# Kernel optimization log

Hardware: AMD Instinct MI355X
Metric: run time of the kernel (lower is better)

## Reference

```python
import jax, jax.numpy as jnp
import numpy as np

S, B, H = 2048, 32, 1024


def setup_inputs() -> dict:
    key = jax.random.key(0)
    k1, k2, k3, k4, k5 = jax.random.split(key, 5)
    scale_w = 1.0 / np.sqrt(2 * H)
    return {
        "hidden": jax.random.normal(k1, (1, B, H), dtype=jnp.float32),
        "encoder_outputs": jax.random.normal(k2, (S, B, H), dtype=jnp.float32),
        "W_attn": jax.random.normal(k3, (H, 2 * H), dtype=jnp.float32) * scale_w,
        "b_attn": jax.random.normal(k4, (H,), dtype=jnp.float32) * scale_w,
        "v": jax.random.normal(k5, (H,), dtype=jnp.float32) * (1.0 / np.sqrt(H)),
    }


def reference(hidden, encoder_outputs, W_attn, b_attn, v):
    # hidden: [1, B, H], encoder_outputs: [S, B, H]
    h = jnp.broadcast_to(hidden, encoder_outputs.shape)          # [S, B, H]
    cat = jnp.concatenate([h, encoder_outputs], axis=2)          # [S, B, 2H]
    alphas = jnp.tanh(jnp.einsum('sbk,hk->sbh', cat, W_attn) + b_attn)  # [S, B, H]
    scores = jnp.einsum('sbh,h->sb', alphas, v)                  # [S, B]
    # softmax over source positions S per batch row, output [B, 1, S]
    return jax.nn.softmax(scores.T, axis=1)[:, None, :]
```

## Files before the change

### kernel.cpp

```cpp
#include <hip/hip_runtime.h>
#include <hip/hip_bf16.h>

typedef unsigned short u16;
typedef unsigned long long u64;
typedef __bf16 bf16x8 __attribute__((ext_vector_type(8)));
typedef float f32x4 __attribute__((ext_vector_type(4)));

#define S_DIM 2048
#define B_DIM 32
#define H_DIM 1024
#define M_DIM (S_DIM * B_DIM)
#define BM 64
#define BKS 32
#define NKS (H_DIM / BKS)

__device__ __forceinline__ float fast_tanh(float x) {
  float e = __expf(2.0f * x);
  return 1.0f - 2.0f * __builtin_amdgcn_rcpf(e + 1.0f);
}

__device__ __forceinline__ void gload_lds16(const void* g, void* l) {
  __builtin_amdgcn_global_load_lds(
      (const __attribute__((address_space(1))) unsigned int*)g,
      (__attribute__((address_space(3))) unsigned int*)l,
      16, 0, 0);
}

__global__ void wconv_kernel(const float* __restrict__ W, u16* __restrict__ W2) {
  const int h = blockIdx.x;
  const int t = threadIdx.x;
  float4 w4 = *(const float4*)(W + (size_t)h * (2 * H_DIM) + H_DIM + t * 4);
  union { u16 s[4]; uint2 v; } pk;
  pk.s[0] = __builtin_bit_cast(u16, (__bf16)w4.x);
  pk.s[1] = __builtin_bit_cast(u16, (__bf16)w4.y);
  pk.s[2] = __builtin_bit_cast(u16, (__bf16)w4.z);
  pk.s[3] = __builtin_bit_cast(u16, (__bf16)w4.w);
  *(uint2*)(W2 + (size_t)h * H_DIM + t * 4) = pk.v;
}

__global__ void uprep_kernel(const float* __restrict__ hidden, const float* __restrict__ W,
                             const float* __restrict__ bias, float* __restrict__ u) {
  int t = blockIdx.x * 256 + threadIdx.x;
  int h = t >> 7;
  int b = (t >> 2) & 31;
  int kq = t & 3;
  const float4* hv = (const float4*)(hidden + (size_t)b * H_DIM) + kq * 64;
  const float4* wv = (const float4*)(W + (size_t)h * (2 * H_DIM)) + kq * 64;
  float acc = 0.f;
  #pragma unroll 4
  for (int i = 0; i < 64; ++i) {
    float4 a = hv[i], w = wv[i];
    acc += a.x * w.x + a.y * w.y + a.z * w.z + a.w * w.w;
  }
  acc += __shfl_xor(acc, 1);
  acc += __shfl_xor(acc, 2);
  if (kq == 0) u[(size_t)b * H_DIM + h] = acc + bias[h];
}

__launch_bounds__(512, 2)
__global__ void gemm_kernel(const float* __restrict__ enc, const u16* __restrict__ W2,
                            const float* __restrict__ u, const float* __restrict__ v,
                            float* __restrict__ scores) {
  __shared__ u16 A_s[2][BM][40];
  __shared__ u16 B_s[2][H_DIM * BKS];
  __shared__ float red_s[8][BM];

  const int tid  = threadIdx.x;
  const int lane = tid & 63;
  const int wid  = tid >> 6;
  const int q    = lane >> 4;
  const int c16  = lane & 15;
  const int n0   = wid * 128;
  const int m0   = blockIdx.x * BM;

  const int ar  = tid >> 3;
  const int acf = tid & 7;
  const float* aptr = enc + (size_t)(m0 + ar) * H_DIM + acf * 4;

  f32x4 acc[4][8];
  #pragma unroll
  for (int mi = 0; mi < 4; ++mi)
    #pragma unroll
    for (int nf = 0; nf < 8; ++nf) {
      f32x4 z = {0.f, 0.f, 0.f, 0.f};
      acc[mi][nf] = z;
    }

  #define STAGE_B(buf, ks)                                                     \
    {                                                                          \
      _Pragma("unroll")                                                        \
      for (int j = 0; j < 8; ++j) {                                            \
        const int L16 = j * 512 + tid;                                         \
        const int h   = L16 >> 2;                                              \
        const int cp  = L16 & 3;                                               \
        const int c   = cp ^ ((h >> 1) & 3);                                   \
        gload_lds16(W2 + (size_t)h * H_DIM + (ks) * BKS + c * 8,               \
                    &B_s[buf][L16 * 8]);                                       \
      }                                                                        \
    }

  #define WRITE_A(buf, f4)                                                     \
    {                                                                          \
      union { u16 s[4]; u64 v; } pk;                                           \
      pk.s[0] = __builtin_bit_cast(u16, (__bf16)(f4).x);                       \
      pk.s[1] = __builtin_bit_cast(u16, (__bf16)(f4).y);                       \
      pk.s[2] = __builtin_bit_cast(u16, (__bf16)(f4).z);                       \
      pk.s[3] = __builtin_bit_cast(u16, (__bf16)(f4).w);                       \
      *(u64*)&A_s[buf][ar][acf * 4] = pk.v;                                    \
    }

  STAGE_B(0, 0);
  {
    float4 a0 = *(const float4*)(aptr);
    WRITE_A(0, a0);
  }
  __syncthreads();

  #pragma unroll 2
  for (int ks = 0; ks < NKS; ++ks) {
    const int cur = ks & 1;
    const int nxt = cur ^ 1;
    float4 av;
    if (ks + 1 < NKS) {
      STAGE_B(nxt, ks + 1);
      av = *(const float4*)(aptr + (ks + 1) * BKS);
    }
    bf16x8 a[4], b[8];
    #pragma unroll
    for (int mi = 0; mi < 4; ++mi)
      a[mi] = *(const bf16x8*)&A_s[cur][mi * 16 + c16][q * 8];
    #pragma unroll
    for (int nf = 0; nf < 8; ++nf) {
      const int col = n0 + nf * 16 + c16;
      b[nf] = *(const bf16x8*)&B_s[cur][col * BKS + ((q ^ ((col >> 1) & 3)) * 8)];
    }
    #pragma unroll
    for (int nf = 0; nf < 8; ++nf)
      #pragma unroll
      for (int mi = 0; mi < 4; ++mi)
        acc[mi][nf] = __builtin_amdgcn_mfma_f32_16x16x32_bf16(a[mi], b[nf], acc[mi][nf], 0, 0, 0);
    if (ks + 1 < NKS) WRITE_A(nxt, av);
    __syncthreads();
  }

  float rowsum[4][4];
  #pragma unroll
  for (int mi = 0; mi < 4; ++mi)
    #pragma unroll
    for (int r = 0; r < 4; ++r) rowsum[mi][r] = 0.f;

  #pragma unroll
  for (int nf = 0; nf < 8; ++nf) {
    const int h = n0 + nf * 16 + c16;
    const float vh = v[h];
    float uv[2][4];
    #pragma unroll
    for (int p = 0; p < 2; ++p)
      #pragma unroll
      for (int r = 0; r < 4; ++r)
        uv[p][r] = u[(size_t)(p * 16 + q * 4 + r) * H_DIM + h];
    #pragma unroll
    for (int mi = 0; mi < 4; ++mi)
      #pragma unroll
      for (int r = 0; r < 4; ++r) {
        float x = acc[mi][nf][r] + uv[mi & 1][r];
        rowsum[mi][r] += vh * fast_tanh(x);
      }
  }
  #pragma unroll
  for (int mi = 0; mi < 4; ++mi)
    #pragma unroll
    for (int r = 0; r < 4; ++r) {
      float s = rowsum[mi][r];
      s += __shfl_xor(s, 1);
      s += __shfl_xor(s, 2);
      s += __shfl_xor(s, 4);
      s += __shfl_xor(s, 8);
      if (c16 == 0) red_s[wid][mi * 16 + q * 4 + r] = s;
    }
  __syncthreads();
  if (tid < BM) {
    float s = 0.f;
    #pragma unroll
    for (int w = 0; w < 8; ++w) s += red_s[w][tid];
    scores[m0 + tid] = s;
  }
  #undef STAGE_B
  #undef WRITE_A
}

__global__ void softmax_kernel(const float* __restrict__ scores, float* __restrict__ out) {
  const int b = blockIdx.x;
  const int t = threadIdx.x;
  const int lane = t & 63, wid = t >> 6;
  __shared__ float redm[4], reds[4];
  float loc[8];
  float mx = -3.0e38f;
  #pragma unroll
  for (int i = 0; i < 8; ++i) {
    loc[i] = scores[(size_t)(i * 256 + t) * B_DIM + b];
    mx = fmaxf(mx, loc[i]);
  }
  #pragma unroll
  for (int off = 1; off < 64; off <<= 1) mx = fmaxf(mx, __shfl_xor(mx, off));
  if (lane == 0) redm[wid] = mx;
  __syncthreads();
  mx = fmaxf(fmaxf(redm[0], redm[1]), fmaxf(redm[2], redm[3]));
  float sum = 0.f;
  #pragma unroll
  for (int i = 0; i < 8; ++i) { loc[i] = __expf(loc[i] - mx); sum += loc[i]; }
  #pragma unroll
  for (int off = 1; off < 64; off <<= 1) sum += __shfl_xor(sum, off);
  if (lane == 0) reds[wid] = sum;
  __syncthreads();
  sum = reds[0] + reds[1] + reds[2] + reds[3];
  float inv = 1.0f / sum;
  #pragma unroll
  for (int i = 0; i < 8; ++i) out[(size_t)b * S_DIM + i * 256 + t] = loc[i] * inv;
}

extern "C" void kernel_launch(void* const* d_in, const int* in_sizes, int n_in,
                              void* d_out, int out_size, void* d_ws, size_t ws_size,
                              hipStream_t stream) {
  const float* hidden = (const float*)d_in[0];
  const float* enc    = (const float*)d_in[1];
  const float* W      = (const float*)d_in[2];
  const float* bias   = (const float*)d_in[3];
  const float* v      = (const float*)d_in[4];
  float* out = (float*)d_out;

  char* ws = (char*)d_ws;
  u16*   W2     = (u16*)ws;
  float* u      = (float*)(ws + (2u << 20));
  float* scores = (float*)(ws + (2u << 20) + (128u << 10));

  wconv_kernel<<<H_DIM, 256, 0, stream>>>(W, W2);
  uprep_kernel<<<512, 256, 0, stream>>>(hidden, W, bias, u);
  gemm_kernel<<<M_DIM / BM, 512, 0, stream>>>(enc, W2, u, v, scores);
  softmax_kernel<<<B_DIM, 256, 0, stream>>>(scores, out);
}
```

Measured before the change: 279.3 us.

## Load W tiles directly into registers instead of staging through LDS

The B operand (bf16 weights) is no longer staged through a 128KB double-buffered LDS array via global_load_lds. Each wave now loads its own B fragments straight from global memory into registers, double-buffered in two register sets. The loop is manually unrolled by two so the register buffers swap at compile time. This cuts LDS traffic and footprint, which may allow more occupancy, but it adds register pressure and issues non-shared global loads. The W tile is re-read per wave and per block, so it depends on L2/L1 hits.

```diff
diff --git a/kernel.cpp b/kernel.cpp
--- a/kernel.cpp
+++ b/kernel.cpp
@@ -17,13 +17,6 @@
 __device__ __forceinline__ float fast_tanh(float x) {
   float e = __expf(2.0f * x);
   return 1.0f - 2.0f * __builtin_amdgcn_rcpf(e + 1.0f);
-}
-
-__device__ __forceinline__ void gload_lds16(const void* g, void* l) {
-  __builtin_amdgcn_global_load_lds(
-      (const __attribute__((address_space(1))) unsigned int*)g,
-      (__attribute__((address_space(3))) unsigned int*)l,
-      16, 0, 0);
 }
 
 __global__ void wconv_kernel(const float* __restrict__ W, u16* __restrict__ W2) {
@@ -62,7 +55,6 @@
                             const float* __restrict__ u, const float* __restrict__ v,
                             float* __restrict__ scores) {
   __shared__ u16 A_s[2][BM][40];
-  __shared__ u16 B_s[2][H_DIM * BKS];
   __shared__ float red_s[8][BM];
 
   const int tid  = threadIdx.x;
@@ -77,6 +69,8 @@
   const int acf = tid & 7;
   const float* aptr = enc + (size_t)(m0 + ar) * H_DIM + acf * 4;
 
+  const u16* wbase = W2 + (size_t)(n0 + c16) * H_DIM + q * 8;
+
   f32x4 acc[4][8];
   #pragma unroll
   for (int mi = 0; mi < 4; ++mi)
@@ -86,17 +80,11 @@
       acc[mi][nf] = z;
     }
 
-  #define STAGE_B(buf, ks)                                                     \
+  #define LOADB(dst, ks)                                                       \
     {                                                                          \
       _Pragma("unroll")                                                        \
-      for (int j = 0; j < 8; ++j) {                                            \
-        const int L16 = j * 512 + tid;                                         \
-        const int h   = L16 >> 2;                                              \
-        const int cp  = L16 & 3;                                               \
-        const int c   = cp ^ ((h >> 1) & 3);                                   \
-        gload_lds16(W2 + (size_t)h * H_DIM + (ks) * BKS + c * 8,               \
-                    &B_s[buf][L16 * 8]);                                       \
-      }                                                                        \
+      for (int nf = 0; nf < 8; ++nf)                                           \
+        dst[nf] = *(const bf16x8*)(wbase + (size_t)nf * 16 * H_DIM + (ks) * BKS); \
     }
 
   #define WRITE_A(buf, f4)                                                     \
@@ -109,38 +97,40 @@
       *(u64*)&A_s[buf][ar][acf * 4] = pk.v;                                    \
     }
 
-  STAGE_B(0, 0);
+  #define KSTEP(ks, BUFC, BCUR, BNXT)                                          \
+    {                                                                          \
+      float4 av;                                                               \
+      const bool pf = (ks) + 1 < NKS;                                          \
+      if (pf) {                                                                \
+        LOADB(BNXT, (ks) + 1);                                                 \
+        av = *(const float4*)(aptr + ((ks) + 1) * BKS);                        \
+      }                                                                        \
+      bf16x8 a[4];                                                             \
+      _Pragma("unroll")                                                        \
+      for (int mi = 0; mi < 4; ++mi)                                           \
+        a[mi] = *(const bf16x8*)&A_s[BUFC][mi * 16 + c16][q * 8];              \
+      _Pragma("unroll")                                                        \
+      for (int nf = 0; nf < 8; ++nf)                                           \
+        _Pragma("unroll")                                                      \
+        for (int mi = 0; mi < 4; ++mi)                                         \
+          acc[mi][nf] = __builtin_amdgcn_mfma_f32_16x16x32_bf16(               \
+              a[mi], BCUR[nf], acc[mi][nf], 0, 0, 0);                          \
+      if (pf) WRITE_A((BUFC) ^ 1, av);                                         \
+      __syncthreads();                                                         \
+    }
+
+  bf16x8 breg0[8], breg1[8];
+  LOADB(breg0, 0);
   {
     float4 a0 = *(const float4*)(aptr);
     WRITE_A(0, a0);
   }
   __syncthreads();
 
-  #pragma unroll 2
-  for (int ks = 0; ks < NKS; ++ks) {
-    const int cur = ks & 1;
-    const int nxt = cur ^ 1;
-    float4 av;
-    if (ks + 1 < NKS) {
-      STAGE_B(nxt, ks + 1);
-      av = *(const float4*)(aptr + (ks + 1) * BKS);
-    }
-    bf16x8 a[4], b[8];
-    #pragma unroll
-    for (int mi = 0; mi < 4; ++mi)
-      a[mi] = *(const bf16x8*)&A_s[cur][mi * 16 + c16][q * 8];
-    #pragma unroll
-    for (int nf = 0; nf < 8; ++nf) {
-      const int col = n0 + nf * 16 + c16;
-      b[nf] = *(const bf16x8*)&B_s[cur][col * BKS + ((q ^ ((col >> 1) & 3)) * 8)];
-    }
-    #pragma unroll
-    for (int nf = 0; nf < 8; ++nf)
-      #pragma unroll
-      for (int mi = 0; mi < 4; ++mi)
-        acc[mi][nf] = __builtin_amdgcn_mfma_f32_16x16x32_bf16(a[mi], b[nf], acc[mi][nf], 0, 0, 0);
-    if (ks + 1 < NKS) WRITE_A(nxt, av);
-    __syncthreads();
+  for (int ks2 = 0; ks2 < NKS / 2; ++ks2) {
+    const int ks = ks2 * 2;
+    KSTEP(ks, 0, breg0, breg1);
+    KSTEP(ks + 1, 1, breg1, breg0);
   }
 
   float rowsum[4][4];
@@ -185,8 +175,9 @@
     for (int w = 0; w < 8; ++w) s += red_s[w][tid];
     scores[m0 + tid] = s;
   }
-  #undef STAGE_B
+  #undef LOADB
   #undef WRITE_A
+  #undef KSTEP
 }
 
 __global__ void softmax_kernel(const float* __restrict__ scores, float* __restrict__ out) {
```

Result: slower. 323.7 us (+15.9%).

## Split GEMM over N into 128x128 tiles with partial-score reduction in softmax

Applied to the files above, without the earlier changes.

Before, each block owned 64 rows and all 1024 output columns. Now the GEMM uses 128x128 tiles with 256-thread blocks, and the N dimension is split into 8 slices. Each slice writes partial v·tanh sums to a workspace, and the softmax kernel adds the 8 partials. The u bias values are staged in LDS. The aim is lower LDS use, higher occupancy and better load balance. In exchange, each 128-row A tile is now loaded once per N slice (8 times instead of once). The B tile also drops its XOR swizzle, which risks LDS bank conflicts.

```diff
diff --git a/kernel.cpp b/kernel.cpp
--- a/kernel.cpp
+++ b/kernel.cpp
@@ -10,9 +10,8 @@
 #define B_DIM 32
 #define H_DIM 1024
 #define M_DIM (S_DIM * B_DIM)
-#define BM 64
-#define BKS 32
-#define NKS (H_DIM / BKS)
+#define NKS 32
+#define NSLICE 8
 
 __device__ __forceinline__ float fast_tanh(float x) {
   float e = __expf(2.0f * x);
@@ -57,91 +56,126 @@
   if (kq == 0) u[(size_t)b * H_DIM + h] = acc + bias[h];
 }
 
-__launch_bounds__(512, 2)
-__global__ void gemm_kernel(const float* __restrict__ enc, const u16* __restrict__ W2,
-                            const float* __restrict__ u, const float* __restrict__ v,
-                            float* __restrict__ scores) {
-  __shared__ u16 A_s[2][BM][40];
-  __shared__ u16 B_s[2][H_DIM * BKS];
-  __shared__ float red_s[8][BM];
+__global__ __launch_bounds__(256, 2)
+void gemm_kernel(const float* __restrict__ enc, const u16* __restrict__ W2,
+                 const float* __restrict__ u, const float* __restrict__ v,
+                 float* __restrict__ partial) {
+  __shared__ u16 A_s[2][4096];
+  __shared__ u16 B_s[2][4096];
+  __shared__ float u_s[32 * 132];
+  __shared__ float red_s[2][128];
 
   const int tid  = threadIdx.x;
   const int lane = tid & 63;
   const int wid  = tid >> 6;
+  const int wm   = wid >> 1;
+  const int wn   = wid & 1;
   const int q    = lane >> 4;
   const int c16  = lane & 15;
-  const int n0   = wid * 128;
-  const int m0   = blockIdx.x * BM;
-
-  const int ar  = tid >> 3;
-  const int acf = tid & 7;
-  const float* aptr = enc + (size_t)(m0 + ar) * H_DIM + acf * 4;
-
-  f32x4 acc[4][8];
+  const int nb   = blockIdx.x & 7;
+  const int mb   = blockIdx.x >> 3;
+  const int m0   = mb * 128;
+  const int n0   = nb * 128;
+
+  f32x4 acc[4][4];
   #pragma unroll
   for (int mi = 0; mi < 4; ++mi)
     #pragma unroll
-    for (int nf = 0; nf < 8; ++nf) {
+    for (int nf = 0; nf < 4; ++nf) {
       f32x4 z = {0.f, 0.f, 0.f, 0.f};
       acc[mi][nf] = z;
     }
 
-  #define STAGE_B(buf, ks)                                                     \
-    {                                                                          \
-      _Pragma("unroll")                                                        \
-      for (int j = 0; j < 8; ++j) {                                            \
-        const int L16 = j * 512 + tid;                                         \
-        const int h   = L16 >> 2;                                              \
-        const int cp  = L16 & 3;                                               \
-        const int c   = cp ^ ((h >> 1) & 3);                                   \
-        gload_lds16(W2 + (size_t)h * H_DIM + (ks) * BKS + c * 8,               \
-                    &B_s[buf][L16 * 8]);                                       \
-      }                                                                        \
-    }
-
-  #define WRITE_A(buf, f4)                                                     \
-    {                                                                          \
-      union { u16 s[4]; u64 v; } pk;                                           \
-      pk.s[0] = __builtin_bit_cast(u16, (__bf16)(f4).x);                       \
-      pk.s[1] = __builtin_bit_cast(u16, (__bf16)(f4).y);                       \
-      pk.s[2] = __builtin_bit_cast(u16, (__bf16)(f4).z);                       \
-      pk.s[3] = __builtin_bit_cast(u16, (__bf16)(f4).w);                       \
-      *(u64*)&A_s[buf][ar][acf * 4] = pk.v;                                    \
+  #pragma unroll
+  for (int jj = 0; jj < 4; ++jj) {
+    const int i  = jj * 1024 + tid * 4;
+    const int b_ = i >> 7, hp = i & 127;
+    float4 uv4 = *(const float4*)(u + (size_t)b_ * H_DIM + n0 + hp);
+    *(float4*)&u_s[b_ * 132 + hp] = uv4;
+  }
+
+  #define STAGE_B(buf, ks)                                                    \
+    {                                                                         \
+      _Pragma("unroll")                                                       \
+      for (int j = 0; j < 2; ++j) {                                           \
+        const int slot = j * 256 + tid;                                       \
+        gload_lds16(W2 + (size_t)(n0 + (slot & 127)) * H_DIM + (ks) * 32 +    \
+                        (slot >> 7) * 8,                                      \
+                    &B_s[buf][slot * 8]);                                     \
+      }                                                                       \
+    }
+
+  #define PACK_WRITE_A(buf, AF)                                               \
+    {                                                                         \
+      _Pragma("unroll")                                                       \
+      for (int j = 0; j < 2; ++j) {                                           \
+        union { u16 s[8]; uint4 vv; } pk;                                     \
+        pk.s[0] = __builtin_bit_cast(u16, (__bf16)AF[j][0].x);                \
+        pk.s[1] = __builtin_bit_cast(u16, (__bf16)AF[j][0].y);                \
+        pk.s[2] = __builtin_bit_cast(u16, (__bf16)AF[j][0].z);                \
+        pk.s[3] = __builtin_bit_cast(u16, (__bf16)AF[j][0].w);                \
+        pk.s[4] = __builtin_bit_cast(u16, (__bf16)AF[j][1].x);                \
+        pk.s[5] = __builtin_bit_cast(u16, (__bf16)AF[j][1].y);                \
+        pk.s[6] = __builtin_bit_cast(u16, (__bf16)AF[j][1].z);                \
+        pk.s[7] = __builtin_bit_cast(u16, (__bf16)AF[j][1].w);                \
+        *(uint4*)&A_s[buf][(j * 256 + tid) * 8] = pk.vv;                      \
+      }                                                                       \
+    }
+
+  #define LOAD_A(AF, ks)                                                      \
+    {                                                                         \
+      _Pragma("unroll")                                                       \
+      for (int j = 0; j < 2; ++j) {                                           \
+        const int task = j * 256 + tid;                                       \
+        const float* ap = enc + (size_t)(m0 + (task & 127)) * H_DIM +         \
+                          (ks) * 32 + (task >> 7) * 8;                        \
+        AF[j][0] = *(const float4*)ap;                                        \
+        AF[j][1] = *(const float4*)(ap + 4);                                  \
+      }                                                                       \
     }
 
   STAGE_B(0, 0);
   {
-    float4 a0 = *(const float4*)(aptr);
-    WRITE_A(0, a0);
-  }
-  __syncthreads();
-
-  #pragma unroll 2
-  for (int ks = 0; ks < NKS; ++ks) {
-    const int cur = ks & 1;
-    const int nxt = cur ^ 1;
-    float4 av;
-    if (ks + 1 < NKS) {
-      STAGE_B(nxt, ks + 1);
-      av = *(const float4*)(aptr + (ks + 1) * BKS);
-    }
-    bf16x8 a[4], b[8];
-    #pragma unroll
-    for (int mi = 0; mi < 4; ++mi)
-      a[mi] = *(const bf16x8*)&A_s[cur][mi * 16 + c16][q * 8];
-    #pragma unroll
-    for (int nf = 0; nf < 8; ++nf) {
-      const int col = n0 + nf * 16 + c16;
-      b[nf] = *(const bf16x8*)&B_s[cur][col * BKS + ((q ^ ((col >> 1) & 3)) * 8)];
-    }
-    #pragma unroll
-    for (int nf = 0; nf < 8; ++nf)
-      #pragma unroll
-      for (int mi = 0; mi < 4; ++mi)
-        acc[mi][nf] = __builtin_amdgcn_mfma_f32_16x16x32_bf16(a[mi], b[nf], acc[mi][nf], 0, 0, 0);
-    if (ks + 1 < NKS) WRITE_A(nxt, av);
-    __syncthreads();
-  }
+    float4 af[2][2];
+    LOAD_A(af, 0);
+    PACK_WRITE_A(0, af);
+  }
+  __syncthreads();
+
+  #define KSTEP(ks, CUR)                                                      \
+    {                                                                         \
+      float4 af[2][2];                                                        \
+      const bool pf = (ks) + 1 < NKS;                                         \
+      if (pf) {                                                               \
+        STAGE_B((CUR) ^ 1, (ks) + 1);                                         \
+        LOAD_A(af, (ks) + 1);                                                 \
+      }                                                                       \
+      bf16x8 a[4], b[4];                                                      \
+      _Pragma("unroll")                                                       \
+      for (int mi = 0; mi < 4; ++mi)                                          \
+        a[mi] = *(const bf16x8*)&A_s[CUR][(q * 128 + wm * 64 + mi * 16 + c16) * 8]; \
+      _Pragma("unroll")                                                       \
+      for (int nf = 0; nf < 4; ++nf)                                          \
+        b[nf] = *(const bf16x8*)&B_s[CUR][(q * 128 + wn * 64 + nf * 16 + c16) * 8]; \
+      _Pragma("unroll")                                                       \
+      for (int nf = 0; nf < 4; ++nf)                                          \
+        _Pragma("unroll")                                                     \
+        for (int mi = 0; mi < 4; ++mi)                                        \
+          acc[mi][nf] = __builtin_amdgcn_mfma_f32_16x16x32_bf16(              \
+              a[mi], b[nf], acc[mi][nf], 0, 0, 0);                            \
+      if (pf) PACK_WRITE_A((CUR) ^ 1, af);                                    \
+      __syncthreads();                                                        \
+    }
+
+  for (int k2 = 0; k2 < NKS / 2; ++k2) {
+    KSTEP(2 * k2, 0);
+    KSTEP(2 * k2 + 1, 1);
+  }
+
+  float vv[4];
+  #pragma unroll
+  for (int nf = 0; nf < 4; ++nf)
+    vv[nf] = v[n0 + wn * 64 + nf * 16 + c16];
 
   float rowsum[4][4];
   #pragma unroll
@@ -150,21 +184,15 @@
     for (int r = 0; r < 4; ++r) rowsum[mi][r] = 0.f;
 
   #pragma unroll
-  for (int nf = 0; nf < 8; ++nf) {
-    const int h = n0 + nf * 16 + c16;
-    const float vh = v[h];
-    float uv[2][4];
-    #pragma unroll
-    for (int p = 0; p < 2; ++p)
-      #pragma unroll
-      for (int r = 0; r < 4; ++r)
-        uv[p][r] = u[(size_t)(p * 16 + q * 4 + r) * H_DIM + h];
+  for (int nf = 0; nf < 4; ++nf) {
+    const int hp = wn * 64 + nf * 16 + c16;
     #pragma unroll
     for (int mi = 0; mi < 4; ++mi)
       #pragma unroll
       for (int r = 0; r < 4; ++r) {
-        float x = acc[mi][nf][r] + uv[mi & 1][r];
-        rowsum[mi][r] += vh * fast_tanh(x);
+        const int b_ = (mi * 16 + q * 4 + r) & 31;
+        float x = acc[mi][nf][r] + u_s[b_ * 132 + hp];
+        rowsum[mi][r] += vv[nf] * fast_tanh(x);
       }
   }
   #pragma unroll
@@ -176,20 +204,22 @@
       s += __shfl_xor(s, 2);
       s += __shfl_xor(s, 4);
       s += __shfl_xor(s, 8);
-      if (c16 == 0) red_s[wid][mi * 16 + q * 4 + r] = s;
-    }
-  __syncthreads();
-  if (tid < BM) {
-    float s = 0.f;
-    #pragma unroll
-    for (int w = 0; w < 8; ++w) s += red_s[w][tid];
-    scores[m0 + tid] = s;
+      if (c16 == 0) red_s[wn][wm * 64 + mi * 16 + q * 4 + r] = s;
+    }
+  __syncthreads();
+  if (tid < 128) {
+    const float sres = red_s[0][tid] + red_s[1][tid];
+    const int b_ = tid & 31;
+    const int s_ = (m0 + tid) >> 5;
+    partial[(size_t)nb * M_DIM + (size_t)b_ * S_DIM + s_] = sres;
   }
   #undef STAGE_B
-  #undef WRITE_A
-}
-
-__global__ void softmax_kernel(const float* __restrict__ scores, float* __restrict__ out) {
+  #undef PACK_WRITE_A
+  #undef LOAD_A
+  #undef KSTEP
+}
+
+__global__ void softmax_kernel(const float* __restrict__ partial, float* __restrict__ out) {
   const int b = blockIdx.x;
   const int t = threadIdx.x;
   const int lane = t & 63, wid = t >> 6;
@@ -198,8 +228,13 @@
   float mx = -3.0e38f;
   #pragma unroll
   for (int i = 0; i < 8; ++i) {
-    loc[i] = scores[(size_t)(i * 256 + t) * B_DIM + b];
-    mx = fmaxf(mx, loc[i]);
+    const int s = i * 256 + t;
+    float a = 0.f;
+    #pragma unroll
+    for (int j = 0; j < NSLICE; ++j)
+      a += partial[(size_t)j * M_DIM + (size_t)b * S_DIM + s];
+    loc[i] = a;
+    mx = fmaxf(mx, a);
   }
   #pragma unroll
   for (int off = 1; off < 64; off <<= 1) mx = fmaxf(mx, __shfl_xor(mx, off));
@@ -230,12 +265,12 @@
   float* out = (float*)d_out;
 
   char* ws = (char*)d_ws;
-  u16*   W2     = (u16*)ws;
-  float* u      = (float*)(ws + (2u << 20));
-  float* scores = (float*)(ws + (2u << 20) + (128u << 10));
+  u16*   W2      = (u16*)ws;
+  float* u       = (float*)(ws + (2u << 20));
+  float* partial = (float*)(ws + (2u << 20) + (128u << 10));
 
   wconv_kernel<<<H_DIM, 256, 0, stream>>>(W, W2);
   uprep_kernel<<<512, 256, 0, stream>>>(hidden, W, bias, u);
-  gemm_kernel<<<M_DIM / BM, 512, 0, stream>>>(enc, W2, u, v, scores);
-  softmax_kernel<<<B_DIM, 256, 0, stream>>>(scores, out);
-}
+  gemm_kernel<<<(M_DIM / 128) * NSLICE, 256, 0, stream>>>(enc, W2, u, v, partial);
+  softmax_kernel<<<B_DIM, 256, 0, stream>>>(partial, out);
+}
```

New measurement: 499.9 us. 1.79x slower.
